# Optimization experiments

Hardware: AMD Instinct MI355X
Metric: run time of the kernel (lower is better)

The kernel has to match this reference:

```python
import jax, jax.numpy as jnp
import numpy as np


def setup_inputs() -> dict:
    key = jax.random.key(0)
    k1, k2 = jax.random.split(key)
    L = 1_000_000  # 1000x1000 meshgrid, flattened
    B = 256        # number of receiver positions
    mesh_2D = jax.random.uniform(k1, (L, 2), dtype=jnp.float32) * 10.0  # room coords in [0,10)m
    receiver_pos = jax.random.uniform(k2, (B, 3), dtype=jnp.float32) * 10.0
    return {"mesh_2D": mesh_2D, "receiver_pos": receiver_pos}


def reference(mesh_2D, receiver_pos):
    # mesh_2D: [L, 2], receiver_pos: [B, 3]
    X = mesh_2D[:, 0]  # [L]
    Y = mesh_2D[:, 1]  # [L]
    # Brute-force receiver-to-mesh squared distances, [B, L].
    # (sqrt is monotone, so argmin over squared distances == argmin over distances)
    d2 = (X[None, :] - receiver_pos[:, 0:1]) ** 2 + (Y[None, :] - receiver_pos[:, 1:2]) ** 2
    min_index = jnp.argmin(d2, axis=1).astype(jnp.int32)  # [B]
    L = X.shape[0]
    one_hot = jnp.zeros((L, 1), dtype=mesh_2D.dtype)
    one_hot = one_hot.at[min_index, 0].set(1.0)
    # Faithful to the torch loop quirk: at iteration k<B-1 the not-yet-filled
    # entries of min_index are 0, so index 0 is also set to 1 whenever B > 1.
    if receiver_pos.shape[0] > 1:
        one_hot = one_hot.at[0, 0].set(1.0)
    closest_points = jnp.stack([X[min_index], Y[min_index]], axis=1)  # [B, 2]
    input_tensor = jnp.concatenate([X[:, None], Y[:, None], one_hot], axis=1).astype(jnp.float32)  # [L, 3]
    return input_tensor, closest_points, min_index
```

## Files before the change

### kernel.cpp

```cpp
#include <hip/hip_runtime.h>
#include <math.h>


#define G      256
#define GG     (G * G)
#define BMW    (GG / 32)
#define CELLW  (10.0f / (float)G)
#define W2     (CELLW * CELLW)
#define GATE   (0.98f * W2)
#define INVW   ((float)G / 10.0f)
#define CAP    64
#define PBASE  ((int)0xAAAAAAAA)
#define FBLK   2048
#define NCHUNK 1024

typedef float f32x4 __attribute__((ext_vector_type(4)));

__device__ __forceinline__ f32x4 ldnt4(const float4* p) {
    return __builtin_nontemporal_load((const f32x4*)p);
}
__device__ __forceinline__ void stnt4(float4* p, float x, float y,
                                      float z, float w) {
    f32x4 v = {x, y, z, w};
    __builtin_nontemporal_store(v, (f32x4*)p);
}

__device__ __forceinline__ int clampi(int v, int lo, int hi) {
    return min(max(v, lo), hi);
}

__device__ __forceinline__ int cell_of(float x, float y) {
    int cx = clampi((int)(x * INVW), 0, G - 1);
    int cy = clampi((int)(y * INVW), 0, G - 1);
    return cy * G + cx;
}


__global__ void filter_copy_kernel(const float4* __restrict__ mesh4,
                                   float4* __restrict__ out4,
                                   const float* __restrict__ recv,
                                   int* __restrict__ cellcnt,
                                   float4* __restrict__ cellbuf,
                                   int L, int B) {
    __shared__ unsigned sbm[BMW];
    int tt = threadIdx.x;

    float rx0 = 0.0f, ry0 = 0.0f;
    const bool hr = (tt < B);
    if (hr) {
        rx0 = recv[3 * tt + 0];
        ry0 = recv[3 * tt + 1];
    }

    for (int i = tt; i < BMW; i += 256) sbm[i] = 0u;
    __syncthreads();

    if (hr) {
        int cx = clampi((int)(rx0 * INVW), 0, G - 1);
        int cy = clampi((int)(ry0 * INVW), 0, G - 1);
        for (int uy = max(cy - 1, 0); uy <= min(cy + 1, G - 1); ++uy)
            for (int ux = max(cx - 1, 0); ux <= min(cx + 1, G - 1); ++ux) {
                int c = uy * G + ux;
                atomicOr(&sbm[c >> 5], 1u << (c & 31));
            }
    }
    for (int r = tt + 256; r < B; r += 256) {
        float rx = recv[3 * r + 0];
        float ry = recv[3 * r + 1];
        int cx = clampi((int)(rx * INVW), 0, G - 1);
        int cy = clampi((int)(ry * INVW), 0, G - 1);
        for (int uy = max(cy - 1, 0); uy <= min(cy + 1, G - 1); ++uy)
            for (int ux = max(cx - 1, 0); ux <= min(cx + 1, G - 1); ++ux) {
                int c = uy * G + ux;
                atomicOr(&sbm[c >> 5], 1u << (c & 31));
            }
    }
    __syncthreads();

    const int nt4 = (L + 3) / 4;
    const int stride = gridDim.x * blockDim.x;
    for (int t = blockIdx.x * blockDim.x + tt; t < nt4; t += stride) {
        int p0 = t * 4;

        float xs[4], ys[4];
        if (p0 + 3 < L) {
            f32x4 a = ldnt4(&mesh4[2 * t]);
            f32x4 b = ldnt4(&mesh4[2 * t + 1]);
            stnt4(&out4[3 * t + 0], a.x, a.y, 0.0f, a.z);
            stnt4(&out4[3 * t + 1], a.w, 0.0f, b.x, b.y);
            stnt4(&out4[3 * t + 2], 0.0f, b.z, b.w, 0.0f);
            xs[0] = a.x; ys[0] = a.y; xs[1] = a.z; ys[1] = a.w;
            xs[2] = b.x; ys[2] = b.y; xs[3] = b.z; ys[3] = b.w;
        } else {
            const float2* mesh = (const float2*)mesh4;
            float* out0 = (float*)out4;
            for (int k = 0; k < 4; ++k) {
                int p = p0 + k;
                if (p >= L) { xs[k] = -100.0f; ys[k] = -100.0f; continue; }
                float2 pt = mesh[p];
                out0[3 * (size_t)p + 0] = pt.x;
                out0[3 * (size_t)p + 1] = pt.y;
                out0[3 * (size_t)p + 2] = 0.0f;
                xs[k] = pt.x; ys[k] = pt.y;
            }
        }

        int c[4];
        unsigned w[4];
        #pragma unroll
        for (int k = 0; k < 4; ++k) c[k] = cell_of(xs[k], ys[k]);
        #pragma unroll
        for (int k = 0; k < 4; ++k) w[k] = sbm[c[k] >> 5];

        #pragma unroll
        for (int k = 0; k < 4; ++k) {
            int p = p0 + k;
            if (p >= L) continue;
            if ((w[k] >> (c[k] & 31)) & 1u) {
                int slot = atomicAdd(&cellcnt[c[k]], 1) - PBASE;
                if (slot >= 0 && slot < CAP) {
                    cellbuf[(size_t)c[k] * CAP + slot] =
                        make_float4(xs[k], ys[k], __int_as_float(p), 0.0f);
                }
            }
        }
    }
}

__global__ __launch_bounds__(256) void argmin_wave_kernel(
        const float2* __restrict__ mesh,
        const float* __restrict__ recv,
        const int* __restrict__ cellcnt,
        const float4* __restrict__ cellbuf,
        float* __restrict__ out0,
        float* __restrict__ out1,
        float* __restrict__ out2,
        int L, int B) {
    const int lane = threadIdx.x & 63;
    const int wid  = threadIdx.x >> 6;
    const int r    = blockIdx.x * 4 + wid;
    if (r >= B) return;

    const float rx = recv[3 * r + 0];
    const float ry = recv[3 * r + 1];
    const int cx = clampi((int)(rx * INVW), 0, G - 1);
    const int cy = clampi((int)(ry * INVW), 0, G - 1);

    int mycell = 0, mycnt = 0, myanom = 0;
    if (lane < 9) {
        int ux = cx + (lane % 3) - 1;
        int uy = cy + (lane / 3) - 1;
        if (ux >= 0 && ux < G && uy >= 0 && uy < G) {
            mycell = uy * G + ux;
            int n = cellcnt[mycell] - PBASE;
            if (n < 0 || n > CAP) { myanom = 1; n = clampi(n, 0, CAP); }
            mycnt = n;
        }
    }
    const int anom = __any(myanom);

    int cc[9], nn[9], bb[10];
    #pragma unroll
    for (int k = 0; k < 9; ++k) {
        cc[k] = __shfl(mycell, k);
        nn[k] = __shfl(mycnt,  k);
    }
    bb[0] = 0;
    #pragma unroll
    for (int k = 0; k < 9; ++k) bb[k + 1] = bb[k] + nn[k];
    const int total = bb[9];

    float bd2 = INFINITY;
    int bidx = 0x7fffffff;
    for (int pos = lane; pos < total; pos += 64) {
        int cell = cc[0], base = bb[0];
        #pragma unroll
        for (int k = 1; k < 9; ++k) {
            if (pos >= bb[k]) { cell = cc[k]; base = bb[k]; }
        }
        float4 e = cellbuf[(size_t)cell * CAP + (pos - base)];
        int pi = __float_as_int(e.z);
        float dx = e.x - rx;
        float dy = e.y - ry;
        float d2 = __fadd_rn(__fmul_rn(dx, dx), __fmul_rn(dy, dy));
        if (d2 < bd2 || (d2 == bd2 && pi < bidx)) { bd2 = d2; bidx = pi; }
    }
    #pragma unroll
    for (int m = 1; m < 64; m <<= 1) {
        float od2 = __shfl_xor(bd2, m);
        int   oi  = __shfl_xor(bidx, m);
        if (od2 < bd2 || (od2 == bd2 && oi < bidx)) { bd2 = od2; bidx = oi; }
    }

    bool ok = (!anom) && (bd2 < GATE) && (bidx >= 0) && (bidx < L);
    if (!ok) {
        bd2 = INFINITY; bidx = 0x7fffffff;
        for (int j = lane; j < L; j += 64) {
            float2 p = mesh[j];
            float dx = p.x - rx;
            float dy = p.y - ry;
            float d2 = __fadd_rn(__fmul_rn(dx, dx), __fmul_rn(dy, dy));
            if (d2 < bd2 || (d2 == bd2 && j < bidx)) { bd2 = d2; bidx = j; }
        }
        #pragma unroll
        for (int m = 1; m < 64; m <<= 1) {
            float od2 = __shfl_xor(bd2, m);
            int   oi  = __shfl_xor(bidx, m);
            if (od2 < bd2 || (od2 == bd2 && oi < bidx)) { bd2 = od2; bidx = oi; }
        }
    }

    if (lane == 0) {
        out2[r] = (float)bidx;
        float2 p = mesh[bidx];
        out1[2 * r + 0] = p.x;
        out1[2 * r + 1] = p.y;
        out0[3 * (size_t)bidx + 2] = 1.0f;
        if (r == 0 && B > 1) out0[2] = 1.0f;
    }
}


__global__ void copy_xy_kernel(const float2* __restrict__ mesh,
                               float* __restrict__ out0, int L) {
    int i = blockIdx.x * blockDim.x + threadIdx.x;
    if (i < L) {
        float2 p = mesh[i];
        out0[3 * i + 0] = p.x;
        out0[3 * i + 1] = p.y;
        out0[3 * i + 2] = 0.0f;
    }
}

__global__ void partial_argmin_kernel(const float2* __restrict__ mesh,
                                      const float* __restrict__ recv,
                                      float* __restrict__ pd2,
                                      int* __restrict__ pidx,
                                      int L, int chunk) {
    const int b = threadIdx.x;
    const int c = blockIdx.x;
    const float rx = recv[3 * b + 0];
    const float ry = recv[3 * b + 1];
    int start = c * chunk;
    int end = min(start + chunk, L);

    float best = INFINITY;
    int bidx = 0x7fffffff;
    #pragma unroll 8
    for (int l = start; l < end; ++l) {
        float2 p = mesh[l];
        float dx = p.x - rx;
        float dy = p.y - ry;
        float d2 = __fadd_rn(__fmul_rn(dx, dx), __fmul_rn(dy, dy));
        if (d2 < best) { best = d2; bidx = l; }
    }
    pd2[c * blockDim.x + b] = best;
    pidx[c * blockDim.x + b] = bidx;
}

__global__ void reduce_finalize_kernel(const float2* __restrict__ mesh,
                                       const float* __restrict__ pd2,
                                       const int* __restrict__ pidx,
                                       float* __restrict__ out0,
                                       float* __restrict__ out1,
                                       float* __restrict__ out2,
                                       int B) {
    const int b = blockIdx.x;
    const int t = threadIdx.x;

    float best = INFINITY;
    int bidx = 0x7fffffff;
    for (int c = t; c < NCHUNK; c += blockDim.x) {
        float d2 = pd2[c * B + b];
        int   i  = pidx[c * B + b];
        if (d2 < best || (d2 == best && i < bidx)) { best = d2; bidx = i; }
    }

    __shared__ float sd[256];
    __shared__ int   si[256];
    sd[t] = best;
    si[t] = bidx;
    __syncthreads();
    for (int s = 128; s > 0; s >>= 1) {
        if (t < s) {
            float d2 = sd[t + s];
            int   i  = si[t + s];
            if (d2 < sd[t] || (d2 == sd[t] && i < si[t])) { sd[t] = d2; si[t] = i; }
        }
        __syncthreads();
    }

    if (t == 0) {
        int idx = si[0];
        out2[b] = (float)idx;
        float2 p = mesh[idx];
        out1[2 * b + 0] = p.x;
        out1[2 * b + 1] = p.y;
        out0[3 * (size_t)idx + 2] = 1.0f;
        if (b == 0) out0[2] = 1.0f;
    }
}

extern "C" void kernel_launch(void* const* d_in, const int* in_sizes, int n_in,
                              void* d_out, int out_size, void* d_ws, size_t ws_size,
                              hipStream_t stream) {
    const float* mesh = (const float*)d_in[0];
    const float* recv = (const float*)d_in[1];
    const int L = in_sizes[0] / 2;
    const int B = in_sizes[1] / 3;

    float* out0 = (float*)d_out;
    float* out1 = out0 + (size_t)3 * L;
    float* out2 = out1 + (size_t)2 * B;

    const size_t need = (size_t)GG * sizeof(int)
                      + (size_t)GG * CAP * sizeof(float4);

    if (ws_size >= need && B <= 4096) {
        int* cellcnt    = (int*)d_ws;
        float4* cellbuf = (float4*)((char*)d_ws + (size_t)GG * sizeof(int));

        filter_copy_kernel<<<FBLK, 256, 0, stream>>>(
            (const float4*)mesh, (float4*)out0, recv, cellcnt, cellbuf, L, B);
        argmin_wave_kernel<<<(B + 3) / 4, 256, 0, stream>>>(
            (const float2*)mesh, recv, cellcnt, cellbuf,
            out0, out1, out2, L, B);
    } else {
        float* pd2  = (float*)d_ws;
        int*   pidx = (int*)((char*)d_ws + sizeof(float) * (size_t)NCHUNK * B);
        const int chunk = (L + NCHUNK - 1) / NCHUNK;

        copy_xy_kernel<<<(L + 255) / 256, 256, 0, stream>>>(
            (const float2*)mesh, out0, L);
        partial_argmin_kernel<<<NCHUNK, B, 0, stream>>>(
            (const float2*)mesh, recv, pd2, pidx, L, chunk);
        reduce_finalize_kernel<<<B, 256, 0, stream>>>(
            (const float2*)mesh, pd2, pidx, out0, out1, out2, B);
    }
}
```

Baseline: 70.96 us.

## Stage interleaved output through LDS for coalesced stores and launch one-shot grid

```diff
diff --git a/kernel.cpp b/kernel.cpp
--- a/kernel.cpp
+++ b/kernel.cpp
@@ -11,7 +11,6 @@
 #define INVW   ((float)G / 10.0f)
 #define CAP    64
 #define PBASE  ((int)0xAAAAAAAA)
-#define FBLK   2048
 #define NCHUNK 1024
 
 typedef float f32x4 __attribute__((ext_vector_type(4)));
@@ -19,9 +18,7 @@
 __device__ __forceinline__ f32x4 ldnt4(const float4* p) {
     return __builtin_nontemporal_load((const f32x4*)p);
 }
-__device__ __forceinline__ void stnt4(float4* p, float x, float y,
-                                      float z, float w) {
-    f32x4 v = {x, y, z, w};
+__device__ __forceinline__ void stnt4(float4* p, f32x4 v) {
     __builtin_nontemporal_store(v, (f32x4*)p);
 }
 
@@ -36,14 +33,16 @@
 }
 
 
-__global__ void filter_copy_kernel(const float4* __restrict__ mesh4,
-                                   float4* __restrict__ out4,
-                                   const float* __restrict__ recv,
-                                   int* __restrict__ cellcnt,
-                                   float4* __restrict__ cellbuf,
-                                   int L, int B) {
+__global__ __launch_bounds__(256) void filter_copy_kernel(
+        const float4* __restrict__ mesh4,
+        float4* __restrict__ out4,
+        const float* __restrict__ recv,
+        int* __restrict__ cellcnt,
+        float4* __restrict__ cellbuf,
+        int L, int B) {
     __shared__ unsigned sbm[BMW];
-    int tt = threadIdx.x;
+    __shared__ float4 stg[3 * 256];
+    const int tt = threadIdx.x;
 
     float rx0 = 0.0f, ry0 = 0.0f;
     const bool hr = (tt < B);
@@ -77,26 +76,32 @@
     }
     __syncthreads();
 
-    const int nt4 = (L + 3) / 4;
-    const int stride = gridDim.x * blockDim.x;
-    for (int t = blockIdx.x * blockDim.x + tt; t < nt4; t += stride) {
-        int p0 = t * 4;
-
-        float xs[4], ys[4];
-        if (p0 + 3 < L) {
+    const int nt4   = (L + 3) / 4;
+    const int nfull = L >> 2;
+    const int t = blockIdx.x * 256 + tt;
+    const bool active = (t < nt4);
+    const bool full   = (t < nfull);
+
+    float xs[4], ys[4];
+    #pragma unroll
+    for (int k = 0; k < 4; ++k) { xs[k] = -100.0f; ys[k] = -100.0f; }
+
+    if (active) {
+        if (full) {
             f32x4 a = ldnt4(&mesh4[2 * t]);
             f32x4 b = ldnt4(&mesh4[2 * t + 1]);
-            stnt4(&out4[3 * t + 0], a.x, a.y, 0.0f, a.z);
-            stnt4(&out4[3 * t + 1], a.w, 0.0f, b.x, b.y);
-            stnt4(&out4[3 * t + 2], 0.0f, b.z, b.w, 0.0f);
+            stg[3 * tt + 0] = make_float4(a.x, a.y, 0.0f, a.z);
+            stg[3 * tt + 1] = make_float4(a.w, 0.0f, b.x, b.y);
+            stg[3 * tt + 2] = make_float4(0.0f, b.z, b.w, 0.0f);
             xs[0] = a.x; ys[0] = a.y; xs[1] = a.z; ys[1] = a.w;
             xs[2] = b.x; ys[2] = b.y; xs[3] = b.z; ys[3] = b.w;
         } else {
             const float2* mesh = (const float2*)mesh4;
             float* out0 = (float*)out4;
+            const int p0 = t * 4;
             for (int k = 0; k < 4; ++k) {
                 int p = p0 + k;
-                if (p >= L) { xs[k] = -100.0f; ys[k] = -100.0f; continue; }
+                if (p >= L) continue;
                 float2 pt = mesh[p];
                 out0[3 * (size_t)p + 0] = pt.x;
                 out0[3 * (size_t)p + 1] = pt.y;
@@ -104,7 +109,24 @@
                 xs[k] = pt.x; ys[k] = pt.y;
             }
         }
-
+    }
+    __syncthreads();
+
+    {
+        const int base3 = blockIdx.x * 768;
+        const int lim3  = 3 * nfull;
+        #pragma unroll
+        for (int k = 0; k < 3; ++k) {
+            int s = tt + 256 * k;
+            int g = base3 + s;
+            if (g < lim3) {
+                f32x4 v = *(const f32x4*)&stg[s];
+                stnt4(&out4[g], v);
+            }
+        }
+    }
+
+    if (active) {
         int c[4];
         unsigned w[4];
         #pragma unroll
@@ -112,6 +134,7 @@
         #pragma unroll
         for (int k = 0; k < 4; ++k) w[k] = sbm[c[k] >> 5];
 
+        const int p0 = t * 4;
         #pragma unroll
         for (int k = 0; k < 4; ++k) {
             int p = p0 + k;
@@ -320,7 +343,10 @@
         int* cellcnt    = (int*)d_ws;
         float4* cellbuf = (float4*)((char*)d_ws + (size_t)GG * sizeof(int));
 
-        filter_copy_kernel<<<FBLK, 256, 0, stream>>>(
+        const int nt4 = (L + 3) / 4;
+        const int nbF = (nt4 + 255) / 256;
+
+        filter_copy_kernel<<<nbF, 256, 0, stream>>>(
             (const float4*)mesh, (float4*)out0, recv, cellcnt, cellbuf, L, B);
         argmin_wave_kernel<<<(B + 3) / 4, 256, 0, stream>>>(
             (const float2*)mesh, recv, cellcnt, cellbuf,
```

New measurement: 69.62 us. Within noise of the previous version (-1.9%).
